# Kernel tuning notes

Hardware: AMD Instinct MI355X
Metric: run time of the kernel (lower is better)

## Reference

```python
import jax, jax.numpy as jnp
import numpy as np

BLK = 128          # stk blocking
HID = 1024         # hidden_size
FFN = 4096         # ffn_hidden_size per expert
NE = 8             # moe_num_experts
TOK = 8192         # padded tokens (multiple of BLK)


def setup_inputs() -> dict:
    key = jax.random.key(0)
    k1, k2, k3 = jax.random.split(key, 3)
    x = jax.random.normal(k1, (TOK, HID), dtype=jnp.float32)
    w1 = jax.random.normal(k2, (NE * FFN, HID), dtype=jnp.float32) * 0.02
    n_row_blocks = TOK // BLK          # 64
    cols_per_expert = FFN // BLK       # 32
    # dMoE topology: each token row-block is assigned one expert; its nonzero
    # column blocks are all ffn blocks of that expert.
    expert_assign = jax.random.randint(k3, (n_row_blocks,), 0, NE)
    row_indices = jnp.repeat(jnp.arange(n_row_blocks), cols_per_expert)
    column_indices = (expert_assign[:, None] * cols_per_expert
                      + jnp.arange(cols_per_expert)[None, :]).reshape(-1)
    return {
        "x": x,
        "w1": w1,
        "row_indices": row_indices.astype(jnp.int32),     # [nnz]
        "column_indices": column_indices.astype(jnp.int32),  # [nnz]
        "block": BLK,
    }


def reference(x, w1, row_indices, column_indices, block):
    # sdd(x, w1.T, topo): out block k = x_block[row_indices[k]] @ w1_block[column_indices[k]].T
    hid = x.shape[1]
    xb = x.reshape(-1, block, hid)    # [n_row_blocks, blk, hid]
    wb = w1.reshape(-1, block, hid)   # [n_col_blocks, blk, hid]
    # [nnz, blk, blk] block-sparse data of the output matrix
    return jnp.einsum('kbh,kch->kbc', xb[row_indices], wb[column_indices])
```

## Files before the change

### kernel.cpp

```cpp
#include <hip/hip_runtime.h>
#include <hip/hip_bf16.h>
#include <stdint.h>

#define HID 1024
#define BLKDIM 128
#define BKT 32
#define NKT (HID / BKT)
#define NBUF 3

using short8 = __attribute__((ext_vector_type(8))) short;
using f32x4  = __attribute__((ext_vector_type(4))) float;
using f32x4v = __attribute__((ext_vector_type(4))) float;

__device__ __forceinline__ uint32_t bfround(float f) {
    uint32_t u = __builtin_bit_cast(uint32_t, f);
    return (u + 0x7FFFu + ((u >> 16) & 1u)) >> 16;
}

__device__ __forceinline__ void gld16(const ushort* g, const ushort* lds_base) {
    __builtin_amdgcn_global_load_lds(
        (const __attribute__((address_space(1))) void*)g,
        (__attribute__((address_space(3))) void*)lds_base, 16, 0, 0);
}

__global__ __launch_bounds__(256)
void cvt_sched_kernel(const float* __restrict__ x, const float* __restrict__ w1,
                      uint4* __restrict__ xb, uint4* __restrict__ wb,
                      int nx8, int nw8,
                      const int* __restrict__ cind, int* __restrict__ perm) {
    const int t = threadIdx.x;
    if (blockIdx.x == 0) {
        __shared__ int er[64], srb[64], goff[9];
        if (t < 64) er[t] = (cind[t * 32] >> 5) & 7;
        __syncthreads();
        if (t == 0) {
            int cnt[8], off[8];
            for (int e = 0; e < 8; ++e) cnt[e] = 0;
            for (int r = 0; r < 64; ++r) cnt[er[r]]++;
            goff[0] = 0;
            for (int e = 0; e < 8; ++e) { goff[e + 1] = goff[e] + cnt[e]; off[e] = goff[e]; }
            for (int r = 0; r < 64; ++r) srb[off[er[r]]++] = r;
        }
        __syncthreads();
        for (int g = t; g < 1024; g += 256) {
            int e = 0;
            while (g >= goff[e + 1] * 16) ++e;
            const int ne = goff[e + 1] - goff[e];
            const int local = g - goff[e] * 16;
            const int j = local / ne;
            const int idx = local - j * ne;
            perm[g] = srb[goff[e] + idx] * 16 + j;
        }
    }
    const int i = blockIdx.x * 256 + t;
    if (i < nx8) {
        const f32x4v* s = reinterpret_cast<const f32x4v*>(x) + (size_t)i * 2;
        f32x4v v0 = __builtin_nontemporal_load(s);
        f32x4v v1 = __builtin_nontemporal_load(s + 1);
        uint4 w;
        w.x = bfround(v0.x) | (bfround(v0.y) << 16);
        w.y = bfround(v0.z) | (bfround(v0.w) << 16);
        w.z = bfround(v1.x) | (bfround(v1.y) << 16);
        w.w = bfround(v1.z) | (bfround(v1.w) << 16);
        xb[i] = w;
    } else if (i < nx8 + nw8) {
        const int j = i - nx8;
        const f32x4v* s = reinterpret_cast<const f32x4v*>(w1) + (size_t)j * 2;
        f32x4v v0 = __builtin_nontemporal_load(s);
        f32x4v v1 = __builtin_nontemporal_load(s + 1);
        uint4 w;
        w.x = bfround(v0.x) | (bfround(v0.y) << 16);
        w.y = bfround(v0.z) | (bfround(v0.w) << 16);
        w.z = bfround(v1.x) | (bfround(v1.y) << 16);
        w.w = bfround(v1.z) | (bfround(v1.w) << 16);
        wb[j] = w;
    }
}

__global__ __launch_bounds__(256, 2)
void sdd_wide_kernel(const ushort* __restrict__ xb, const ushort* __restrict__ wb,
                     const int* __restrict__ rind, const int* __restrict__ cind,
                     const int* __restrict__ perm,
                     float* __restrict__ out) {
    __shared__ ushort lds[NBUF * BLKDIM * BKT + NBUF * 2 * BLKDIM * BKT];

    int g = blockIdx.x;
    const int nwg = gridDim.x;
    if ((nwg & 7) == 0) {
        const int cpx = nwg >> 3;
        g = (g & 7) * cpx + (g >> 3);
    }
    g = perm[g];
    const int k0 = g * 2;
    const int r  = rind[k0];

    const int t = threadIdx.x;
    const int w = t >> 6;
    const int l = t & 63;

    ushort* sAb = lds;
    ushort* sBb = lds + NBUF * BLKDIM * BKT;

    const int unx   = (l & 7) ^ ((l >> 3) & 7);
    const int rin16 = 2 * (l >> 3) + (unx >> 2);
    const int kofs  = (unx & 3) * 8;

    const ushort* agb = xb + (size_t)(r * BLKDIM + w * 32 + rin16) * HID + kofs;
    const int cblk = cind[k0 + (w >> 1)];
    const ushort* bgb = wb + (size_t)(cblk * BLKDIM + (w & 1) * 64 + rin16) * HID + kofs;

    const int wr   = (w >> 1) * 64;
    const int wblk = w & 1;
    const int ps_l = (((l >> 4) + ((l & 1) << 2)) ^ ((l & 15) >> 1)) * 8;
    const int rhalf = (l & 15) >> 1;

    int aoff[4], boff[8];
#pragma unroll
    for (int m = 0; m < 4; ++m) aoff[m] = ((w >> 1) * 32 + m * 8 + rhalf) * 64 + ps_l;
#pragma unroll
    for (int n = 0; n < 8; ++n) boff[n] = (wblk * 64 + n * 8 + rhalf) * 64 + ps_l;

    f32x4 acc[4][8];
#pragma unroll
    for (int m = 0; m < 4; ++m)
#pragma unroll
        for (int n = 0; n < 8; ++n)
            acc[m][n] = (f32x4){0.f, 0.f, 0.f, 0.f};

    auto stage = [&](int b, int kt) {
        gld16(agb + kt * BKT,                          &sAb[b * 4096 + w * 1024]);
        gld16(agb + (size_t)16 * HID + kt * BKT,       &sAb[b * 4096 + w * 1024 + 512]);
        gld16(bgb + kt * BKT,                          &sBb[b * 8192 + w * 2048]);
        gld16(bgb + (size_t)16 * HID + kt * BKT,       &sBb[b * 8192 + w * 2048 + 512]);
        gld16(bgb + (size_t)32 * HID + kt * BKT,       &sBb[b * 8192 + w * 2048 + 1024]);
        gld16(bgb + (size_t)48 * HID + kt * BKT,       &sBb[b * 8192 + w * 2048 + 1536]);
    };

    stage(0, 0);
    stage(1, 1);
    asm volatile("s_waitcnt vmcnt(6)" ::: "memory");
    __builtin_amdgcn_s_barrier();
    __builtin_amdgcn_sched_barrier(0);

    for (int kt = 0; kt < NKT; ++kt) {
        const int cur = kt % 3;
        const int nxt = (kt + 2) % 3;
        const bool pre = (kt + 2) < NKT;
        const ushort* sa = &sAb[cur * 4096];
        const ushort* sb = &sBb[cur * 8192];

        short8 aF[4], bF[8];
#pragma unroll
        for (int m = 0; m < 4; ++m)
            aF[m] = *reinterpret_cast<const short8*>(&sa[aoff[m]]);
#pragma unroll
        for (int n = 0; n < 8; ++n)
            bF[n] = *reinterpret_cast<const short8*>(&sb[boff[n]]);
        if (pre) stage(nxt, kt + 2);
        __builtin_amdgcn_s_setprio(1);
#pragma unroll
        for (int m = 0; m < 4; ++m)
#pragma unroll
            for (int n = 0; n < 8; ++n)
                acc[m][n] = __builtin_amdgcn_mfma_f32_16x16x32_bf16(aF[m], bF[n], acc[m][n], 0, 0, 0);
        __builtin_amdgcn_s_setprio(0);

        if (pre) asm volatile("s_waitcnt vmcnt(6)" ::: "memory");
        else     asm volatile("s_waitcnt vmcnt(0)" ::: "memory");
        __builtin_amdgcn_s_barrier();
        __builtin_amdgcn_sched_barrier(0);
    }

    float* op = out + (size_t)(k0 + wblk) * (BLKDIM * BLKDIM);
    float* scr = reinterpret_cast<float*>(lds) + w * 1216;

#pragma unroll
    for (int m = 0; m < 4; ++m)
#pragma unroll
        for (int h = 0; h < 2; ++h) {
#pragma unroll
            for (int n = 0; n < 4; ++n)
#pragma unroll
                for (int j = 0; j < 4; ++j)
                    scr[((l >> 4) * 4 + j) * 76 + n * 16 + (l & 15)] = acc[m][h * 4 + n][j];
#pragma unroll
            for (int rg = 0; rg < 4; ++rg) {
                const int tr = rg * 4 + (l >> 4);
                f32x4 v = *reinterpret_cast<const f32x4*>(&scr[tr * 76 + (l & 15) * 4]);
                __builtin_nontemporal_store(v,
                    reinterpret_cast<f32x4*>(&op[(size_t)(wr + m * 16 + tr) * BLKDIM
                                                 + h * 64 + (l & 15) * 4]));
            }
        }
}

__device__ __forceinline__ void store16f(ushort* dst, float4 v0, float4 v1, float4 v2, float4 v3) {
    uint4 w0, w1;
    w0.x = bfround(v0.x) | (bfround(v0.y) << 16);
    w0.y = bfround(v0.z) | (bfround(v0.w) << 16);
    w0.z = bfround(v1.x) | (bfround(v1.y) << 16);
    w0.w = bfround(v1.z) | (bfround(v1.w) << 16);
    w1.x = bfround(v2.x) | (bfround(v2.y) << 16);
    w1.y = bfround(v2.z) | (bfround(v2.w) << 16);
    w1.z = bfround(v3.x) | (bfround(v3.y) << 16);
    w1.w = bfround(v3.z) | (bfround(v3.w) << 16);
    uint4* d = reinterpret_cast<uint4*>(dst);
    d[0] = w0; d[1] = w1;
}

__global__ __launch_bounds__(256, 2)
void sdd_bf16_kernel(const float* __restrict__ x, const float* __restrict__ w1,
                     const int* __restrict__ rind, const int* __restrict__ cind,
                     float* __restrict__ out) {
    __shared__ ushort sA[2][BLKDIM * 32];
    __shared__ ushort sB[2][BLKDIM * 32];
    const int k = blockIdx.x;
    const int t = threadIdx.x;
    const int r = rind[k];
    const int c = cind[k];
    const float* Abase = x  + (size_t)r * BLKDIM * HID;
    const float* Bbase = w1 + (size_t)c * BLKDIM * HID;
    const int srow = t >> 1, shalf = t & 1;
    const float* aptr = Abase + (size_t)srow * HID + shalf * 16;
    const float* bptr = Bbase + (size_t)srow * HID + shalf * 16;
    const int soff = srow * 32 + shalf * 16;
    const int wv = t >> 6, lane = t & 63;
    const int wr = (wv >> 1) * 64, wc = (wv & 1) * 64;
    const int lr = lane & 15, lk = (lane >> 4) * 8;
    f32x4 acc[4][4];
#pragma unroll
    for (int m = 0; m < 4; ++m)
#pragma unroll
        for (int n = 0; n < 4; ++n) acc[m][n] = (f32x4){0.f, 0.f, 0.f, 0.f};
    float4 ra[4], rb[4];
#pragma unroll
    for (int i = 0; i < 4; ++i) {
        ra[i] = *reinterpret_cast<const float4*>(aptr + i * 4);
        rb[i] = *reinterpret_cast<const float4*>(bptr + i * 4);
    }
    store16f(&sA[0][soff], ra[0], ra[1], ra[2], ra[3]);
    store16f(&sB[0][soff], rb[0], rb[1], rb[2], rb[3]);
    __syncthreads();
    for (int kt = 0; kt < 32; ++kt) {
        const int cur = kt & 1;
        if (kt + 1 < 32) {
            const float* ap = aptr + (kt + 1) * 32;
            const float* bp = bptr + (kt + 1) * 32;
#pragma unroll
            for (int i = 0; i < 4; ++i) {
                ra[i] = *reinterpret_cast<const float4*>(ap + i * 4);
                rb[i] = *reinterpret_cast<const float4*>(bp + i * 4);
            }
        }
        const ushort* sa = sA[cur];
        const ushort* sb = sB[cur];
        short8 aF[4], bF[4];
#pragma unroll
        for (int m = 0; m < 4; ++m) aF[m] = *reinterpret_cast<const short8*>(&sa[(wr + m * 16 + lr) * 32 + lk]);
#pragma unroll
        for (int n = 0; n < 4; ++n) bF[n] = *reinterpret_cast<const short8*>(&sb[(wc + n * 16 + lr) * 32 + lk]);
#pragma unroll
        for (int m = 0; m < 4; ++m)
#pragma unroll
            for (int n = 0; n < 4; ++n)
                acc[m][n] = __builtin_amdgcn_mfma_f32_16x16x32_bf16(aF[m], bF[n], acc[m][n], 0, 0, 0);
        if (kt + 1 < 32) {
            store16f(&sA[cur ^ 1][soff], ra[0], ra[1], ra[2], ra[3]);
            store16f(&sB[cur ^ 1][soff], rb[0], rb[1], rb[2], rb[3]);
        }
        __syncthreads();
    }
    float* op = out + (size_t)k * (BLKDIM * BLKDIM);
    const int rbase = wr + (lane >> 4) * 4;
#pragma unroll
    for (int m = 0; m < 4; ++m)
#pragma unroll
        for (int n = 0; n < 4; ++n) {
            const int col = wc + n * 16 + lr;
#pragma unroll
            for (int j = 0; j < 4; ++j)
                op[(size_t)(rbase + m * 16 + j) * BLKDIM + col] = acc[m][n][j];
        }
}

extern "C" void kernel_launch(void* const* d_in, const int* in_sizes, int n_in,
                              void* d_out, int out_size, void* d_ws, size_t ws_size,
                              hipStream_t stream) {
    const float* x  = (const float*)d_in[0];
    const float* w1 = (const float*)d_in[1];
    const int* ri   = (const int*)d_in[2];
    const int* ci   = (const int*)d_in[3];
    float* out      = (float*)d_out;
    const int nnz   = in_sizes[2];
    const int nx    = in_sizes[0];
    const int nw    = in_sizes[1];

    const size_t need = ((size_t)nx + (size_t)nw) * sizeof(ushort) + 4096 * sizeof(int);
    if (ws_size >= need && nnz == 2048 && nx == 8388608 && nw == 33554432) {
        ushort* xb = (ushort*)d_ws;
        ushort* wb = xb + nx;
        int* perm  = (int*)(wb + nw);
        const int nx8 = nx / 8, nw8 = nw / 8;
        const int ncvt = (nx8 + nw8 + 255) / 256;
        hipLaunchKernelGGL(cvt_sched_kernel, dim3(ncvt), dim3(256), 0, stream,
                           x, w1, (uint4*)xb, (uint4*)wb, nx8, nw8, ci, perm);
        hipLaunchKernelGGL(sdd_wide_kernel, dim3(nnz / 2), dim3(256), 0, stream,
                           xb, wb, ri, ci, perm, out);
    } else {
        hipLaunchKernelGGL(sdd_bf16_kernel, dim3(nnz), dim3(256), 0, stream,
                           x, w1, ri, ci, out);
    }
}
```

Before: 123.3 us.

## Load fp32 weights directly into LDS and convert to bf16 in GEMM loop

Drops the separate pass that converts all of w1 to bf16. The GEMM kernel now streams fp32 weight tiles into LDS and rounds them to bf16 while building the MFMA operands. This saves a full read and write of the 128MB weight tensor, and weights for experts that are never selected are no longer touched. In exchange, each kernel reads twice the bytes for B, does conversion ALU work in the inner loop, and drops from triple to double buffering with an extra barrier per k-step.

```diff
diff --git a/kernel.cpp b/kernel.cpp
--- a/kernel.cpp
+++ b/kernel.cpp
@@ -6,7 +6,6 @@
 #define BLKDIM 128
 #define BKT 32
 #define NKT (HID / BKT)
-#define NBUF 3
 
 using short8 = __attribute__((ext_vector_type(8))) short;
 using f32x4  = __attribute__((ext_vector_type(4))) float;
@@ -22,11 +21,14 @@
         (const __attribute__((address_space(1))) void*)g,
         (__attribute__((address_space(3))) void*)lds_base, 16, 0, 0);
 }
+__device__ __forceinline__ void gld16f(const float* g, const float* lds_base) {
+    __builtin_amdgcn_global_load_lds(
+        (const __attribute__((address_space(1))) void*)g,
+        (__attribute__((address_space(3))) void*)lds_base, 16, 0, 0);
+}
 
 __global__ __launch_bounds__(256)
-void cvt_sched_kernel(const float* __restrict__ x, const float* __restrict__ w1,
-                      uint4* __restrict__ xb, uint4* __restrict__ wb,
-                      int nx8, int nw8,
+void cvt_sched_kernel(const float* __restrict__ x, uint4* __restrict__ xb, int nx8,
                       const int* __restrict__ cind, int* __restrict__ perm) {
     const int t = threadIdx.x;
     if (blockIdx.x == 0) {
@@ -63,26 +65,16 @@
         w.z = bfround(v1.x) | (bfround(v1.y) << 16);
         w.w = bfround(v1.z) | (bfround(v1.w) << 16);
         xb[i] = w;
-    } else if (i < nx8 + nw8) {
-        const int j = i - nx8;
-        const f32x4v* s = reinterpret_cast<const f32x4v*>(w1) + (size_t)j * 2;
-        f32x4v v0 = __builtin_nontemporal_load(s);
-        f32x4v v1 = __builtin_nontemporal_load(s + 1);
-        uint4 w;
-        w.x = bfround(v0.x) | (bfround(v0.y) << 16);
-        w.y = bfround(v0.z) | (bfround(v0.w) << 16);
-        w.z = bfround(v1.x) | (bfround(v1.y) << 16);
-        w.w = bfround(v1.z) | (bfround(v1.w) << 16);
-        wb[j] = w;
     }
 }
 
 __global__ __launch_bounds__(256, 2)
-void sdd_wide_kernel(const ushort* __restrict__ xb, const ushort* __restrict__ wb,
+void sdd_bf32_kernel(const ushort* __restrict__ xb, const float* __restrict__ w1,
                      const int* __restrict__ rind, const int* __restrict__ cind,
                      const int* __restrict__ perm,
                      float* __restrict__ out) {
-    __shared__ ushort lds[NBUF * BLKDIM * BKT + NBUF * 2 * BLKDIM * BKT];
+    __shared__ ushort sA[2][BLKDIM * BKT];
+    __shared__ float  sB[2][256 * BKT];
 
     int g = blockIdx.x;
     const int nwg = gridDim.x;
@@ -98,27 +90,33 @@
     const int w = t >> 6;
     const int l = t & 63;
 
-    ushort* sAb = lds;
-    ushort* sBb = lds + NBUF * BLKDIM * BKT;
-
     const int unx   = (l & 7) ^ ((l >> 3) & 7);
     const int rin16 = 2 * (l >> 3) + (unx >> 2);
     const int kofs  = (unx & 3) * 8;
-
     const ushort* agb = xb + (size_t)(r * BLKDIM + w * 32 + rin16) * HID + kofs;
+
+    const int slog = (l & 7) ^ (l >> 3);
     const int cblk = cind[k0 + (w >> 1)];
-    const ushort* bgb = wb + (size_t)(cblk * BLKDIM + (w & 1) * 64 + rin16) * HID + kofs;
-
+    const float* bgf = w1 + (size_t)(cblk * BLKDIM + (w & 1) * 64 + (l >> 3)) * HID + slog * 4;
+
+    const int wblk = w & 1;
     const int wr   = (w >> 1) * 64;
-    const int wblk = w & 1;
-    const int ps_l = (((l >> 4) + ((l & 1) << 2)) ^ ((l & 15) >> 1)) * 8;
-    const int rhalf = (l & 15) >> 1;
-
-    int aoff[4], boff[8];
+    const int lr   = l & 15;
+    const int ps_l = (((l >> 4) + ((l & 1) << 2)) ^ (lr >> 1)) * 8;
+    const int rhalf = lr >> 1;
+
+    int aoff[4];
 #pragma unroll
     for (int m = 0; m < 4; ++m) aoff[m] = ((w >> 1) * 32 + m * 8 + rhalf) * 64 + ps_l;
-#pragma unroll
-    for (int n = 0; n < 8; ++n) boff[n] = (wblk * 64 + n * 8 + rhalf) * 64 + ps_l;
+
+    const int p0 = ((l >> 4) * 2) ^ (lr & 7);
+    int bo0[8], bo1[8];
+#pragma unroll
+    for (int n = 0; n < 8; ++n) {
+        const int base = (wblk * 128 + n * 16 + lr) * 32;
+        bo0[n] = base + p0 * 4;
+        bo1[n] = base + (p0 ^ 1) * 4;
+    }
 
     f32x4 acc[4][8];
 #pragma unroll
@@ -127,36 +125,49 @@
         for (int n = 0; n < 8; ++n)
             acc[m][n] = (f32x4){0.f, 0.f, 0.f, 0.f};
 
-    auto stage = [&](int b, int kt) {
-        gld16(agb + kt * BKT,                          &sAb[b * 4096 + w * 1024]);
-        gld16(agb + (size_t)16 * HID + kt * BKT,       &sAb[b * 4096 + w * 1024 + 512]);
-        gld16(bgb + kt * BKT,                          &sBb[b * 8192 + w * 2048]);
-        gld16(bgb + (size_t)16 * HID + kt * BKT,       &sBb[b * 8192 + w * 2048 + 512]);
-        gld16(bgb + (size_t)32 * HID + kt * BKT,       &sBb[b * 8192 + w * 2048 + 1024]);
-        gld16(bgb + (size_t)48 * HID + kt * BKT,       &sBb[b * 8192 + w * 2048 + 1536]);
+    auto stageA = [&](int b, int kt) {
+        gld16(agb + kt * BKT,                    &sA[b][w * 1024]);
+        gld16(agb + (size_t)16 * HID + kt * BKT, &sA[b][w * 1024 + 512]);
     };
-
-    stage(0, 0);
-    stage(1, 1);
-    asm volatile("s_waitcnt vmcnt(6)" ::: "memory");
+    auto stageB = [&](int b, int kt) {
+#pragma unroll
+        for (int i = 0; i < 8; ++i)
+            gld16f(bgf + (size_t)(i * 8) * HID + kt * BKT, &sB[b][(w * 64 + i * 8) * 32]);
+    };
+
+    stageA(0, 0); stageB(0, 0);
+    stageA(1, 1); stageB(1, 1);
+    asm volatile("s_waitcnt vmcnt(10)" ::: "memory");
     __builtin_amdgcn_s_barrier();
     __builtin_amdgcn_sched_barrier(0);
 
     for (int kt = 0; kt < NKT; ++kt) {
-        const int cur = kt % 3;
-        const int nxt = (kt + 2) % 3;
-        const bool pre = (kt + 2) < NKT;
-        const ushort* sa = &sAb[cur * 4096];
-        const ushort* sb = &sBb[cur * 8192];
+        const int cur = kt & 1;
+        const ushort* sa = sA[cur];
+        const float*  sbf = sB[cur];
 
         short8 aF[4], bF[8];
 #pragma unroll
         for (int m = 0; m < 4; ++m)
             aF[m] = *reinterpret_cast<const short8*>(&sa[aoff[m]]);
 #pragma unroll
-        for (int n = 0; n < 8; ++n)
-            bF[n] = *reinterpret_cast<const short8*>(&sb[boff[n]]);
-        if (pre) stage(nxt, kt + 2);
+        for (int n = 0; n < 8; ++n) {
+            f32x4 lo = *reinterpret_cast<const f32x4*>(&sbf[bo0[n]]);
+            f32x4 hi = *reinterpret_cast<const f32x4*>(&sbf[bo1[n]]);
+            uint4 u;
+            u.x = bfround(lo.x) | (bfround(lo.y) << 16);
+            u.y = bfround(lo.z) | (bfround(lo.w) << 16);
+            u.z = bfround(hi.x) | (bfround(hi.y) << 16);
+            u.w = bfround(hi.z) | (bfround(hi.w) << 16);
+            bF[n] = __builtin_bit_cast(short8, u);
+        }
+        asm volatile("s_waitcnt lgkmcnt(0)" ::: "memory");
+        __builtin_amdgcn_sched_barrier(0);
+        __builtin_amdgcn_s_barrier();
+        __builtin_amdgcn_sched_barrier(0);
+
+        if (kt + 2 < NKT) { stageA(cur, kt + 2); stageB(cur, kt + 2); }
+
         __builtin_amdgcn_s_setprio(1);
 #pragma unroll
         for (int m = 0; m < 4; ++m)
@@ -165,14 +176,16 @@
                 acc[m][n] = __builtin_amdgcn_mfma_f32_16x16x32_bf16(aF[m], bF[n], acc[m][n], 0, 0, 0);
         __builtin_amdgcn_s_setprio(0);
 
-        if (pre) asm volatile("s_waitcnt vmcnt(6)" ::: "memory");
-        else     asm volatile("s_waitcnt vmcnt(0)" ::: "memory");
+        if (kt + 1 < NKT) {
+            if (kt + 2 < NKT) asm volatile("s_waitcnt vmcnt(10)" ::: "memory");
+            else              asm volatile("s_waitcnt vmcnt(0)"  ::: "memory");
+        }
         __builtin_amdgcn_s_barrier();
         __builtin_amdgcn_sched_barrier(0);
     }
 
     float* op = out + (size_t)(k0 + wblk) * (BLKDIM * BLKDIM);
-    float* scr = reinterpret_cast<float*>(lds) + w * 1216;
+    float* scr = &sB[0][0] + w * 1216;
 
 #pragma unroll
     for (int m = 0; m < 4; ++m)
@@ -182,14 +195,14 @@
             for (int n = 0; n < 4; ++n)
 #pragma unroll
                 for (int j = 0; j < 4; ++j)
-                    scr[((l >> 4) * 4 + j) * 76 + n * 16 + (l & 15)] = acc[m][h * 4 + n][j];
+                    scr[((l >> 4) * 4 + j) * 76 + n * 16 + lr] = acc[m][h * 4 + n][j];
 #pragma unroll
             for (int rg = 0; rg < 4; ++rg) {
                 const int tr = rg * 4 + (l >> 4);
-                f32x4 v = *reinterpret_cast<const f32x4*>(&scr[tr * 76 + (l & 15) * 4]);
+                f32x4 v = *reinterpret_cast<const f32x4*>(&scr[tr * 76 + lr * 4]);
                 __builtin_nontemporal_store(v,
                     reinterpret_cast<f32x4*>(&op[(size_t)(wr + m * 16 + tr) * BLKDIM
-                                                 + h * 64 + (l & 15) * 4]));
+                                                 + h * 64 + lr * 4]));
             }
         }
 }
@@ -295,17 +308,15 @@
     const int nx    = in_sizes[0];
     const int nw    = in_sizes[1];
 
-    const size_t need = ((size_t)nx + (size_t)nw) * sizeof(ushort) + 4096 * sizeof(int);
+    const size_t need = (size_t)nx * sizeof(ushort) + 1024 * sizeof(int);
     if (ws_size >= need && nnz == 2048 && nx == 8388608 && nw == 33554432) {
         ushort* xb = (ushort*)d_ws;
-        ushort* wb = xb + nx;
-        int* perm  = (int*)(wb + nw);
-        const int nx8 = nx / 8, nw8 = nw / 8;
-        const int ncvt = (nx8 + nw8 + 255) / 256;
-        hipLaunchKernelGGL(cvt_sched_kernel, dim3(ncvt), dim3(256), 0, stream,
-                           x, w1, (uint4*)xb, (uint4*)wb, nx8, nw8, ci, perm);
-        hipLaunchKernelGGL(sdd_wide_kernel, dim3(nnz / 2), dim3(256), 0, stream,
-                           xb, wb, ri, ci, perm, out);
+        int* perm  = (int*)(xb + nx);
+        const int nx8 = nx / 8;
+        hipLaunchKernelGGL(cvt_sched_kernel, dim3((nx8 + 255) / 256), dim3(256), 0, stream,
+                           x, (uint4*)xb, nx8, ci, perm);
+        hipLaunchKernelGGL(sdd_bf32_kernel, dim3(nnz / 2), dim3(256), 0, stream,
+                           xb, w1, ri, ci, perm, out);
     } else {
         hipLaunchKernelGGL(sdd_bf16_kernel, dim3(nnz), dim3(256), 0, stream,
                            x, w1, ri, ci, out);
```

Measured after the change: 130.2 us. +5.6%, slower.
